# Kernel optimization log

Hardware: AMD Instinct MI355X
Metric: run time of the kernel (lower is better)

Reference implementation:

```python
import jax, jax.numpy as jnp
import numpy as np
from jax import lax

B, T, H, E, V, ENC = 2048, 48, 512, 256, 128, 1024


def setup_inputs() -> dict:
    key = jax.random.key(0)
    ks = jax.random.split(key, 13)
    s = 0.05  # weight scale to keep activations sane
    return {
        "tgt_ids": jax.random.randint(ks[0], (B, T), 0, V),
        "enc_hid": jax.random.normal(ks[1], (B, ENC), jnp.float32),
        "W_init1": s * jax.random.normal(ks[2], (ENC, H), jnp.float32),
        "W_init2": s * jax.random.normal(ks[3], (ENC, H), jnp.float32),
        "embed_table": s * jax.random.normal(ks[4], (V, E), jnp.float32),
        "k1": s * jax.random.normal(ks[5], (E, 3 * H), jnp.float32),
        "rk1": s * jax.random.normal(ks[6], (H, 3 * H), jnp.float32),
        "b1": jnp.zeros((2, 3 * H), jnp.float32),
        "k2": s * jax.random.normal(ks[7], (H, 3 * H), jnp.float32),
        "rk2": s * jax.random.normal(ks[8], (H, 3 * H), jnp.float32),
        "b2": jnp.zeros((2, 3 * H), jnp.float32),
        "Wv": s * jax.random.normal(ks[9], (H, V), jnp.float32),
        "bv": jnp.zeros((V,), jnp.float32),
    }


def gru_masked(x_proj, mask, h0, rk, rb):
    """Keras GRU (reset_after=True, gate order z,r,h) with mask carry-through.
    x_proj: [B,T,3H] precomputed x@kernel + input_bias. mask: [B,T] bool.
    Masked steps keep previous state AND previous output (Keras masking semantics;
    GRU output == state)."""
    def step(h, inp):
        xg, m = inp  # xg: [B,3H], m: [B]
        inner = h @ rk + rb  # [B,3H]
        xz, xr, xh = jnp.split(xg, 3, axis=-1)
        rz, rr, rh = jnp.split(inner, 3, axis=-1)
        z = jax.nn.sigmoid(xz + rz)
        r = jax.nn.sigmoid(xr + rr)
        hh = jnp.tanh(xh + r * rh)
        h_new = z * h + (1.0 - z) * hh
        h = jnp.where(m[:, None], h_new, h)
        return h, h

    _, seq = lax.scan(step, h0, (x_proj.transpose(1, 0, 2), mask.T))
    return seq.transpose(1, 0, 2)  # [B,T,H]


def reference(tgt_ids, enc_hid, W_init1, W_init2, embed_table,
              k1, rk1, b1, k2, rk2, b2, Wv, bv):
    mask = tgt_ids != 0  # mask_zero=True
    emb = embed_table[tgt_ids]  # [B,T,E]
    h01 = enc_hid @ W_init1  # Dense no-bias init of layer-1 state
    h02 = enc_hid @ W_init2
    x1 = emb @ k1 + b1[0]  # [B,T,3H]
    seq1 = gru_masked(x1, mask, h01, rk1, b1[1])
    x2 = seq1 @ k2 + b2[0]
    seq2 = gru_masked(x2, mask, h02, rk2, b2[1])
    probs = jax.nn.softmax(seq2 @ Wv + bv, axis=-1)  # [B,T,V]
    return probs
```

## Files before the change

kernel.cpp:

```cpp
#include <hip/hip_runtime.h>
#include <hip/hip_bf16.h>
#include <math.h>

#define B_   2048
#define T_   48
#define H_   512
#define E_   256
#define V_   128
#define ENC_ 1024
#define H3_  1536
#define BH_  (B_ * H_)
#define NBLK_ 512

typedef __attribute__((ext_vector_type(8))) short bf16x8;
typedef __attribute__((ext_vector_type(4))) float f32x4;
typedef unsigned short ushort_t;

#if defined(__has_builtin)
#if __has_builtin(__builtin_amdgcn_global_load_lds)
#define HAVE_ASYNC 1
#endif
#endif
#ifndef HAVE_ASYNC
#define HAVE_ASYNC 0
#endif

__device__ __forceinline__ void stage16(const ushort_t* g, ushort_t* l, int lane)
{
#if HAVE_ASYNC
    __builtin_amdgcn_global_load_lds(
        (const __attribute__((address_space(1))) unsigned int*)g,
        (__attribute__((address_space(3))) unsigned int*)l, 16, 0, 0);
#else
    *(bf16x8*)(l + lane * 8) = *(const bf16x8*)g;
#endif
}

__device__ __forceinline__ float sigmoidf_(float x) { return 1.0f / (1.0f + expf(-x)); }

__device__ __forceinline__ void tile_map(int lin, int& m0, int& i0)
{
    i0 = ((((lin & 7) << 1) | ((lin >> 3) & 1))) * 32;
    m0 = (lin >> 4) * 64;
}

constexpr int BM = 64, BN = 64, BK = 16;

__global__ __launch_bounds__(256) void gemm_f32(
    const float* __restrict__ A, const float* __restrict__ Bm,
    const float* __restrict__ bias, float* __restrict__ C,
    int M, int N, int K)
{
    __shared__ float As[BK][BM + 4];
    __shared__ float Bs[BK][BN + 4];

    const int tid = threadIdx.x;
    const int bm = blockIdx.y * BM;
    const int bn = blockIdx.x * BN;
    const int tm = (tid >> 4) * 4;
    const int tn = (tid & 15) * 4;
    const int lmA = tid >> 2;
    const int lkA = (tid & 3) * 4;
    const int lkB = tid >> 4;
    const int lnB = (tid & 15) * 4;

    float acc[4][4] = {};

    for (int k0 = 0; k0 < K; k0 += BK) {
        float4 av  = *(const float4*)(A  + (size_t)(bm + lmA) * K + (k0 + lkA));
        float4 bv4 = *(const float4*)(Bm + (size_t)(k0 + lkB) * N + (bn + lnB));
        As[lkA + 0][lmA] = av.x;
        As[lkA + 1][lmA] = av.y;
        As[lkA + 2][lmA] = av.z;
        As[lkA + 3][lmA] = av.w;
        *(float4*)&Bs[lkB][lnB] = bv4;
        __syncthreads();

        #pragma unroll
        for (int k = 0; k < BK; ++k) {
            float4 a = *(const float4*)&As[k][tm];
            float4 b = *(const float4*)&Bs[k][tn];
            acc[0][0] += a.x * b.x; acc[0][1] += a.x * b.y; acc[0][2] += a.x * b.z; acc[0][3] += a.x * b.w;
            acc[1][0] += a.y * b.x; acc[1][1] += a.y * b.y; acc[1][2] += a.y * b.z; acc[1][3] += a.y * b.w;
            acc[2][0] += a.z * b.x; acc[2][1] += a.z * b.y; acc[2][2] += a.z * b.z; acc[2][3] += a.z * b.w;
            acc[3][0] += a.w * b.x; acc[3][1] += a.w * b.y; acc[3][2] += a.w * b.z; acc[3][3] += a.w * b.w;
        }
        __syncthreads();
    }

    #pragma unroll
    for (int r = 0; r < 4; ++r)
        #pragma unroll
        for (int c = 0; c < 4; ++c) {
            float v = acc[r][c];
            if (bias) v += bias[bn + tn + c];
            C[(size_t)(bm + tm + r) * N + (bn + tn + c)] = v;
        }
}

__global__ __launch_bounds__(256) void transpose_to_bf16(
    const float* __restrict__ W, __hip_bfloat16* __restrict__ Wt, int K, int N)
{
    __shared__ float tile[32][33];
    const int bk = blockIdx.y * 32, bn = blockIdx.x * 32;
    const int tx = threadIdx.x & 31, ty = threadIdx.x >> 5;
    #pragma unroll
    for (int i = ty; i < 32; i += 8)
        tile[i][tx] = W[(size_t)(bk + i) * N + (bn + tx)];
    __syncthreads();
    #pragma unroll
    for (int i = ty; i < 32; i += 8)
        Wt[(size_t)(bn + i) * K + (bk + tx)] = __float2bfloat16(tile[tx][i]);
}

__global__ __launch_bounds__(256) void transpose_split(
    const float* __restrict__ W, __hip_bfloat16* __restrict__ Whi,
    __hip_bfloat16* __restrict__ Wlo, int K, int N)
{
    __shared__ float tile[32][33];
    const int bk = blockIdx.y * 32, bn = blockIdx.x * 32;
    const int tx = threadIdx.x & 31, ty = threadIdx.x >> 5;
    #pragma unroll
    for (int i = ty; i < 32; i += 8)
        tile[i][tx] = W[(size_t)(bk + i) * N + (bn + tx)];
    __syncthreads();
    #pragma unroll
    for (int i = ty; i < 32; i += 8) {
        const float v = tile[tx][i];
        const __hip_bfloat16 h = __float2bfloat16(v);
        Whi[(size_t)(bn + i) * K + (bk + tx)] = h;
        Wlo[(size_t)(bn + i) * K + (bk + tx)] = __float2bfloat16(v - __bfloat162float(h));
    }
}

__global__ __launch_bounds__(256) void split_cast(
    const float* __restrict__ x, __hip_bfloat16* __restrict__ hi,
    __hip_bfloat16* __restrict__ lo, int n)
{
    const int i0 = (blockIdx.x * 256 + threadIdx.x) * 4;
    if (i0 >= n) return;
    const float4 v = *(const float4*)(x + i0);
    const float vv[4] = { v.x, v.y, v.z, v.w };
    #pragma unroll
    for (int j = 0; j < 4; ++j) {
        const __hip_bfloat16 h = __float2bfloat16(vv[j]);
        hi[i0 + j] = h;
        lo[i0 + j] = __float2bfloat16(vv[j] - __bfloat162float(h));
    }
}

__global__ __launch_bounds__(256, 2) void init_mfma(
    const ushort_t* __restrict__ ehi, const ushort_t* __restrict__ elo,
    const ushort_t* __restrict__ w1hi, const ushort_t* __restrict__ w1lo,
    const ushort_t* __restrict__ w2hi, const ushort_t* __restrict__ w2lo,
    float* __restrict__ h1f, __hip_bfloat16* __restrict__ h1b,
    float* __restrict__ h2f, __hip_bfloat16* __restrict__ h2b)
{
    const ushort_t* whi = blockIdx.z ? w2hi : w1hi;
    const ushort_t* wlo = blockIdx.z ? w2lo : w1lo;
    float* hf = blockIdx.z ? h2f : h1f;
    __hip_bfloat16* hb = blockIdx.z ? h2b : h1b;

    __shared__ __attribute__((aligned(16))) ushort_t Ahi[2][4096];
    __shared__ __attribute__((aligned(16))) ushort_t Alo[2][4096];
    __shared__ __attribute__((aligned(16))) ushort_t Bhi[2][2048];
    __shared__ __attribute__((aligned(16))) ushort_t Blo[2][2048];

    const int tid  = threadIdx.x;
    const int lane = tid & 63;
    const int w    = tid >> 6;
    const int ln   = lane & 15;
    const int kg   = lane >> 4;
    const int wr   = w >> 1, wc = w & 1;
    const int m0   = blockIdx.y * 64;
    const int i0   = blockIdx.x * 32;

    const int crow = lane >> 3;
    const int ckof = ((lane & 7) ^ crow) * 8;
    const int ko0 = (kg * 8) ^ ((ln & 7) * 8);
    const int ko1 = (32 + kg * 8) ^ ((ln & 7) * 8);

    auto STG = [&](int pb, int k0) {
        #pragma unroll
        for (int c = w; c < 24; c += 4) {
            const ushort_t* g; ushort_t* l;
            if (c < 8) {
                g = ehi + (size_t)(m0 + c * 8 + crow) * ENC_ + k0 + ckof;
                l = &Ahi[pb][c * 512];
            } else if (c < 16) {
                const int cc = c - 8;
                g = elo + (size_t)(m0 + cc * 8 + crow) * ENC_ + k0 + ckof;
                l = &Alo[pb][cc * 512];
            } else if (c < 20) {
                const int cc = c - 16;
                g = whi + (size_t)(i0 + cc * 8 + crow) * ENC_ + k0 + ckof;
                l = &Bhi[pb][cc * 512];
            } else {
                const int cc = c - 20;
                g = wlo + (size_t)(i0 + cc * 8 + crow) * ENC_ + k0 + ckof;
                l = &Blo[pb][cc * 512];
            }
            stage16(g, l, lane);
        }
    };

    f32x4 acc[2] = {};
    STG(0, 0);
    __syncthreads();
    int buf = 0;
    for (int k0 = 0; k0 < ENC_; k0 += 64) {
        if (k0 + 64 < ENC_) STG(buf ^ 1, k0 + 64);
        #pragma unroll
        for (int kk = 0; kk < 2; ++kk) {
            const int ko = kk ? ko1 : ko0;
            bf16x8 ah[2], al[2], bh, bl;
            #pragma unroll
            for (int fm = 0; fm < 2; ++fm) {
                ah[fm] = *(const bf16x8*)(&Ahi[buf][(wr * 32 + fm * 16 + ln) * 64 + ko]);
                al[fm] = *(const bf16x8*)(&Alo[buf][(wr * 32 + fm * 16 + ln) * 64 + ko]);
            }
            bh = *(const bf16x8*)(&Bhi[buf][(wc * 16 + ln) * 64 + ko]);
            bl = *(const bf16x8*)(&Blo[buf][(wc * 16 + ln) * 64 + ko]);
            #pragma unroll
            for (int fm = 0; fm < 2; ++fm) {
                acc[fm] = __builtin_amdgcn_mfma_f32_16x16x32_bf16(ah[fm], bh, acc[fm], 0, 0, 0);
                acc[fm] = __builtin_amdgcn_mfma_f32_16x16x32_bf16(al[fm], bh, acc[fm], 0, 0, 0);
                acc[fm] = __builtin_amdgcn_mfma_f32_16x16x32_bf16(ah[fm], bl, acc[fm], 0, 0, 0);
            }
        }
        __syncthreads();
        buf ^= 1;
    }

    const int i = i0 + wc * 16 + ln;
    #pragma unroll
    for (int fm = 0; fm < 2; ++fm)
        #pragma unroll
        for (int r = 0; r < 4; ++r) {
            const int b = m0 + wr * 32 + fm * 16 + kg * 4 + r;
            const float v = acc[fm][r];
            hf[(size_t)b * H_ + i] = v;
            hb[(size_t)b * H_ + i] = __float2bfloat16(v);
        }
}

template<int MODE>
__device__ __forceinline__ void fused_phase(
    ushort_t* lds, int m0, int i0, int i, int t1, int t2,
    const int* __restrict__ tgt, const float* __restrict__ xe1,
    const ushort_t* __restrict__ rk1t,
    float rbz, float rbr, float rbh,
    const ushort_t* __restrict__ k2t, const ushort_t* __restrict__ rk2t,
    float bxz, float bxr, float bxh, float brz, float brr, float brh,
    const ushort_t* __restrict__ h1cur,
    const ushort_t* __restrict__ h2cur, size_t h2s,
    __hip_bfloat16* __restrict__ h1nxt,
    __hip_bfloat16* __restrict__ sout, size_t souts,
    float (&hv1)[2][4], float (&hv2)[2][4])
{
    ushort_t* A1l = lds;
    ushort_t* A2l = lds + 8192;
    ushort_t* B1l = lds + 16384;
    ushort_t* B2l = lds + 22528;
    ushort_t* B3l = lds + 28672;

    const int tid = threadIdx.x, lane = tid & 63, w = tid >> 6;
    const int ln = lane & 15, kg = lane >> 4, wr = w >> 1;
    const int crow = lane >> 3;
    const int ckof = ((lane & 7) ^ crow) * 8;
    const int ko0 = (kg * 8) ^ ((ln & 7) * 8);
    const int ko1 = (32 + kg * 8) ^ ((ln & 7) * 8);

    int ids1[2][4], ids2[2][4];
    float xgz[2][4], xgr[2][4], xgh[2][4];
    #pragma unroll
    for (int fm = 0; fm < 2; ++fm)
        #pragma unroll
        for (int r = 0; r < 4; ++r) {
            const int b = m0 + wr * 32 + fm * 16 + kg * 4 + r;
            if (MODE != 2) ids1[fm][r] = tgt[(size_t)b * T_ + t1];
            if (MODE != 1) ids2[fm][r] = tgt[(size_t)b * T_ + t2];
        }
    if (MODE != 2) {
        #pragma unroll
        for (int fm = 0; fm < 2; ++fm)
            #pragma unroll
            for (int r = 0; r < 4; ++r) {
                const float* xg = xe1 + (size_t)ids1[fm][r] * H3_;
                xgz[fm][r] = xg[i]; xgr[fm][r] = xg[H_ + i]; xgh[fm][r] = xg[2 * H_ + i];
            }
    }

    constexpr int NA = (MODE == 1) ? 8 : 16;
    constexpr int NB = (MODE == 0) ? 36 : ((MODE == 1) ? 12 : 24);

    auto STAGE_A = [&](int pb, int k0) {
        #pragma unroll
        for (int c = w; c < NA; c += 4) {
            const ushort_t* g; ushort_t* l;
            if (c < 8) {
                g = h1cur + (size_t)(m0 + c * 8 + crow) * H_ + k0 + ckof;
                l = A1l + pb * 4096 + c * 512;
            } else {
                const int cc = c - 8;
                g = h2cur + (size_t)(m0 + cc * 8 + crow) * h2s + k0 + ckof;
                l = A2l + pb * 4096 + cc * 512;
            }
            stage16(g, l, lane);
        }
    };
    auto STAGE_B = [&](int k0) {
        #pragma unroll
        for (int c = w; c < NB; c += 4) {
            const ushort_t* g; ushort_t* l;
            if (MODE == 1) {
                g = rk1t + (size_t)((c >> 2) * H_ + i0 + (c & 3) * 8 + crow) * H_ + k0 + ckof;
                l = B1l + c * 512;
            } else if (MODE == 2) {
                if (c < 12) {
                    g = k2t + (size_t)((c >> 2) * H_ + i0 + (c & 3) * 8 + crow) * H_ + k0 + ckof;
                    l = B2l + c * 512;
                } else {
                    const int d = c - 12;
                    g = rk2t + (size_t)((d >> 2) * H_ + i0 + (d & 3) * 8 + crow) * H_ + k0 + ckof;
                    l = B3l + d * 512;
                }
            } else {
                if (c < 12) {
                    g = rk1t + (size_t)((c >> 2) * H_ + i0 + (c & 3) * 8 + crow) * H_ + k0 + ckof;
                    l = B1l + c * 512;
                } else if (c < 24) {
                    const int d = c - 12;
                    g = k2t + (size_t)((d >> 2) * H_ + i0 + (d & 3) * 8 + crow) * H_ + k0 + ckof;
                    l = B2l + d * 512;
                } else {
                    const int d = c - 24;
                    g = rk2t + (size_t)((d >> 2) * H_ + i0 + (d & 3) * 8 + crow) * H_ + k0 + ckof;
                    l = B3l + d * 512;
                }
            }
            stage16(g, l, lane);
        }
    };

    f32x4 acc1[2][3] = {};
    f32x4 accx[2][3] = {};
    f32x4 accr[2][3] = {};

    STAGE_A(0, 0);
    STAGE_B(0);
    __syncthreads();
    int buf = 0;
    for (int k0 = 0; k0 < H_; k0 += 64) {
        const bool more = (k0 + 64 < H_);
        if (more) STAGE_A(buf ^ 1, k0 + 64);

        bf16x8 a1f[2][2], a2f[2][2], b1f[2][3], b2f[2][3], b3f[2][3];
        #pragma unroll
        for (int kk = 0; kk < 2; ++kk) {
            const int ko = kk ? ko1 : ko0;
            #pragma unroll
            for (int fm = 0; fm < 2; ++fm) {
                a1f[kk][fm] = *(const bf16x8*)(A1l + buf * 4096 + (wr * 32 + fm * 16 + ln) * 64 + ko);
                if (MODE != 1)
                    a2f[kk][fm] = *(const bf16x8*)(A2l + buf * 4096 + (wr * 32 + fm * 16 + ln) * 64 + ko);
            }
            #pragma unroll
            for (int g = 0; g < 3; ++g) {
                if (MODE != 2)
                    b1f[kk][g] = *(const bf16x8*)(B1l + g * 2048 + ((w & 1) * 16 + ln) * 64 + ko);
                if (MODE != 1) {
                    b2f[kk][g] = *(const bf16x8*)(B2l + g * 2048 + ((w & 1) * 16 + ln) * 64 + ko);
                    b3f[kk][g] = *(const bf16x8*)(B3l + g * 2048 + ((w & 1) * 16 + ln) * 64 + ko);
                }
            }
        }
        __builtin_amdgcn_sched_barrier(0);
        asm volatile("s_waitcnt lgkmcnt(0)" ::: "memory");
        __builtin_amdgcn_sched_barrier(0);
        __builtin_amdgcn_s_barrier();
        if (more) STAGE_B(k0 + 64);

        #pragma unroll
        for (int kk = 0; kk < 2; ++kk)
            #pragma unroll
            for (int fm = 0; fm < 2; ++fm)
                #pragma unroll
                for (int g = 0; g < 3; ++g) {
                    if (MODE != 2)
                        acc1[fm][g] = __builtin_amdgcn_mfma_f32_16x16x32_bf16(
                            a1f[kk][fm], b1f[kk][g], acc1[fm][g], 0, 0, 0);
                    if (MODE != 1) {
                        accx[fm][g] = __builtin_amdgcn_mfma_f32_16x16x32_bf16(
                            a1f[kk][fm], b2f[kk][g], accx[fm][g], 0, 0, 0);
                        accr[fm][g] = __builtin_amdgcn_mfma_f32_16x16x32_bf16(
                            a2f[kk][fm], b3f[kk][g], accr[fm][g], 0, 0, 0);
                    }
                }
        __syncthreads();
        buf ^= 1;
    }

    if (MODE != 2) {
        #pragma unroll
        for (int fm = 0; fm < 2; ++fm)
            #pragma unroll
            for (int r = 0; r < 4; ++r) {
                const int b = m0 + wr * 32 + fm * 16 + kg * 4 + r;
                const float hvv = hv1[fm][r];
                float z  = sigmoidf_(xgz[fm][r] + acc1[fm][0][r] + rbz);
                float rr = sigmoidf_(xgr[fm][r] + acc1[fm][1][r] + rbr);
                float hh = tanhf(xgh[fm][r] + rr * (acc1[fm][2][r] + rbh));
                float hn = (ids1[fm][r] != 0) ? (z * hvv + (1.0f - z) * hh) : hvv;
                hv1[fm][r] = hn;
                h1nxt[(size_t)b * H_ + i] = __float2bfloat16(hn);
            }
    }
    if (MODE != 1) {
        #pragma unroll
        for (int fm = 0; fm < 2; ++fm)
            #pragma unroll
            for (int r = 0; r < 4; ++r) {
                const int b = m0 + wr * 32 + fm * 16 + kg * 4 + r;
                const float hvv = hv2[fm][r];
                float z  = sigmoidf_((accx[fm][0][r] + bxz) + (accr[fm][0][r] + brz));
                float rr = sigmoidf_((accx[fm][1][r] + bxr) + (accr[fm][1][r] + brr));
                float hh = tanhf((accx[fm][2][r] + bxh) + rr * (accr[fm][2][r] + brh));
                float hn = (ids2[fm][r] != 0) ? (z * hvv + (1.0f - z) * hh) : hvv;
                hv2[fm][r] = hn;
                sout[(size_t)b * souts + i] = __float2bfloat16(hn);
            }
    }
}

__global__ __launch_bounds__(256, 2) void l1_fused(
    const int* __restrict__ tgt, int t,
    const float* __restrict__ xe1, const ushort_t* __restrict__ rkt,
    const float* __restrict__ rb,
    const float* __restrict__ hf_cur, const ushort_t* __restrict__ hb_cur,
    float* __restrict__ hf_nxt, __hip_bfloat16* __restrict__ hb_nxt)
{
    __shared__ __attribute__((aligned(16))) ushort_t lds[34816];
    int m0, i0; tile_map(blockIdx.x, m0, i0);
    const int tid = threadIdx.x, lane = tid & 63, w = tid >> 6;
    const int ln = lane & 15, kg = lane >> 4, wr = w >> 1, wc = w & 1;
    const int i = i0 + wc * 16 + ln;

    float hv1[2][4], hv2[2][4];
    #pragma unroll
    for (int fm = 0; fm < 2; ++fm)
        #pragma unroll
        for (int r = 0; r < 4; ++r)
            hv1[fm][r] = hf_cur[(size_t)(m0 + wr * 32 + fm * 16 + kg * 4 + r) * H_ + i];

    fused_phase<1>(lds, m0, i0, i, t, 0, tgt, xe1, rkt,
                   rb[i], rb[H_ + i], rb[2 * H_ + i],
                   nullptr, nullptr, 0.f, 0.f, 0.f, 0.f, 0.f, 0.f,
                   hb_cur, nullptr, 0, hb_nxt, nullptr, 0, hv1, hv2);

    #pragma unroll
    for (int fm = 0; fm < 2; ++fm)
        #pragma unroll
        for (int r = 0; r < 4; ++r)
            hf_nxt[(size_t)(m0 + wr * 32 + fm * 16 + kg * 4 + r) * H_ + i] = hv1[fm][r];
}

__global__ __launch_bounds__(256, 2) void l2_fused(
    const int* __restrict__ tgt, int t,
    const ushort_t* __restrict__ k2t, const ushort_t* __restrict__ rk2t,
    const float* __restrict__ bx, const float* __restrict__ br,
    const ushort_t* __restrict__ s1b,
    const float* __restrict__ hf_cur,
    const ushort_t* __restrict__ hb_cur, size_t hbs,
    float* __restrict__ hf_nxt,
    __hip_bfloat16* __restrict__ hbo, size_t hos)
{
    __shared__ __attribute__((aligned(16))) ushort_t lds[34816];
    int m0, i0; tile_map(blockIdx.x, m0, i0);
    const int tid = threadIdx.x, lane = tid & 63, w = tid >> 6;
    const int ln = lane & 15, kg = lane >> 4, wr = w >> 1, wc = w & 1;
    const int i = i0 + wc * 16 + ln;

    float hv1[2][4], hv2[2][4];
    #pragma unroll
    for (int fm = 0; fm < 2; ++fm)
        #pragma unroll
        for (int r = 0; r < 4; ++r)
            hv2[fm][r] = hf_cur[(size_t)(m0 + wr * 32 + fm * 16 + kg * 4 + r) * H_ + i];

    fused_phase<2>(lds, m0, i0, i, 0, t, tgt, nullptr, nullptr,
                   0.f, 0.f, 0.f,
                   k2t, rk2t,
                   bx[i], bx[H_ + i], bx[2 * H_ + i],
                   br[i], br[H_ + i], br[2 * H_ + i],
                   s1b, hb_cur, hbs, nullptr, hbo, hos, hv1, hv2);

    #pragma unroll
    for (int fm = 0; fm < 2; ++fm)
        #pragma unroll
        for (int r = 0; r < 4; ++r)
            hf_nxt[(size_t)(m0 + wr * 32 + fm * 16 + kg * 4 + r) * H_ + i] = hv2[fm][r];
}

__device__ __forceinline__ void grid_barrier(unsigned* bar, unsigned phase)
{
    __syncthreads();
    if (threadIdx.x == 0) {
        __builtin_amdgcn_fence(__ATOMIC_RELEASE, "agent");
        const unsigned arrived =
            __hip_atomic_fetch_add(&bar[0], 1u, __ATOMIC_RELAXED, __HIP_MEMORY_SCOPE_AGENT) + 1u;
        if (arrived == (unsigned)NBLK_ * (phase + 1u)) {
            __hip_atomic_store(&bar[1], phase + 1u, __ATOMIC_RELAXED, __HIP_MEMORY_SCOPE_AGENT);
        } else {
            while (__hip_atomic_load(&bar[1], __ATOMIC_RELAXED, __HIP_MEMORY_SCOPE_AGENT) < phase + 1u)
                __builtin_amdgcn_s_sleep(4);
        }
        __builtin_amdgcn_fence(__ATOMIC_ACQUIRE, "agent");
    }
    __syncthreads();
}

__global__ __launch_bounds__(256, 2) void recurrence_all(
    const int* __restrict__ tgt, const float* __restrict__ xe1,
    const ushort_t* __restrict__ rk1t, const float* __restrict__ rb1,
    const ushort_t* __restrict__ k2t, const ushort_t* __restrict__ rk2t,
    const float* __restrict__ bx, const float* __restrict__ br,
    const float* __restrict__ h1f0, __hip_bfloat16* __restrict__ h1b,
    const float* __restrict__ h2f0, const __hip_bfloat16* __restrict__ h2b0,
    __hip_bfloat16* __restrict__ seq2b, unsigned* __restrict__ bar)
{
    __shared__ __attribute__((aligned(16))) ushort_t lds[34816];
    int m0, i0; tile_map(blockIdx.x, m0, i0);
    const int tid = threadIdx.x, lane = tid & 63, w = tid >> 6;
    const int ln = lane & 15, kg = lane >> 4, wr = w >> 1, wc = w & 1;
    const int i = i0 + wc * 16 + ln;

    const float rbz = rb1[i], rbr = rb1[H_ + i], rbh = rb1[2 * H_ + i];
    const float bxz = bx[i],  bxr = bx[H_ + i],  bxh = bx[2 * H_ + i];
    const float brz = br[i],  brr = br[H_ + i],  brh = br[2 * H_ + i];

    float hv1[2][4], hv2[2][4];
    #pragma unroll
    for (int fm = 0; fm < 2; ++fm)
        #pragma unroll
        for (int r = 0; r < 4; ++r) {
            const size_t b = (size_t)(m0 + wr * 32 + fm * 16 + kg * 4 + r) * H_ + i;
            hv1[fm][r] = h1f0[b];
            hv2[fm][r] = h2f0[b];
        }

    unsigned ph = 0;

    fused_phase<1>(lds, m0, i0, i, 0, 0, tgt, xe1, rk1t, rbz, rbr, rbh,
                   nullptr, nullptr, 0.f, 0.f, 0.f, 0.f, 0.f, 0.f,
                   (const ushort_t*)h1b, nullptr, 0, h1b + BH_, nullptr, 0,
                   hv1, hv2);
    grid_barrier(bar, ph); ++ph;

    #pragma unroll 1
    for (int p = 0; p < T_ - 1; ++p) {
        const ushort_t* s1 = (const ushort_t*)(h1b + (size_t)((p + 1) & 1) * BH_);
        const ushort_t* a2 = (p == 0) ? (const ushort_t*)h2b0
                                      : (const ushort_t*)(seq2b + (size_t)(p - 1) * H_);
        const size_t a2s = (p == 0) ? (size_t)H_ : (size_t)T_ * H_;

        fused_phase<0>(lds, m0, i0, i, p + 1, p, tgt, xe1, rk1t, rbz, rbr, rbh,
                       k2t, rk2t, bxz, bxr, bxh, brz, brr, brh,
                       s1, a2, a2s,
                       h1b + (size_t)(p & 1) * BH_,
                       seq2b + (size_t)p * H_, (size_t)T_ * H_,
                       hv1, hv2);
        grid_barrier(bar, ph); ++ph;
    }

    {
        const int p = T_ - 1;
        const ushort_t* s1 = (const ushort_t*)(h1b + (size_t)((p + 1) & 1) * BH_);
        const ushort_t* a2 = (const ushort_t*)(seq2b + (size_t)(p - 1) * H_);
        fused_phase<2>(lds, m0, i0, i, 0, p, tgt, nullptr, nullptr, 0.f, 0.f, 0.f,
                       k2t, rk2t, bxz, bxr, bxh, brz, brr, brh,
                       s1, a2, (size_t)T_ * H_,
                       nullptr, seq2b + (size_t)p * H_, (size_t)T_ * H_,
                       hv1, hv2);
    }
}

__device__ __forceinline__ void softmax_write4(
    float ax, float ay, float az, float aw, float* __restrict__ outp, int cg)
{
    float m = fmaxf(fmaxf(ax, ay), fmaxf(az, aw));
    #pragma unroll
    for (int d = 16; d >= 1; d >>= 1) m = fmaxf(m, __shfl_xor(m, d));
    float ex = __expf(ax - m), ey = __expf(ay - m),
          ez = __expf(az - m), ew = __expf(aw - m);
    float s = ex + ey + ez + ew;
    #pragma unroll
    for (int d = 16; d >= 1; d >>= 1) s += __shfl_xor(s, d);
    float inv = 1.0f / s;
    float4 o; o.x = ex * inv; o.y = ey * inv; o.z = ez * inv; o.w = ew * inv;
    *(float4*)(outp + cg * 4) = o;
}

__global__ __launch_bounds__(256) void out_softmax(
    const float* __restrict__ h2, const float* __restrict__ Wv,
    const float* __restrict__ bv, float* __restrict__ out, int t)
{
    const int tid = threadIdx.x;
    const int cg = tid & 31;
    const int rg = tid >> 5;
    const int row0 = blockIdx.x * 16;

    __shared__ float hs[16][512];
    for (int idx = tid; idx < 16 * 512; idx += 256)
        hs[idx >> 9][idx & 511] = h2[(size_t)(row0 + (idx >> 9)) * 512 + (idx & 511)];
    __syncthreads();

    const int r0 = rg * 2;
    const float4 bvv = *(const float4*)(bv + cg * 4);
    float a0x = bvv.x, a0y = bvv.y, a0z = bvv.z, a0w = bvv.w;
    float a1x = bvv.x, a1y = bvv.y, a1z = bvv.z, a1w = bvv.w;

    #pragma unroll 4
    for (int k = 0; k < 512; ++k) {
        float4 wv = *(const float4*)(Wv + (size_t)k * V_ + cg * 4);
        float h0 = hs[r0][k], h1 = hs[r0 + 1][k];
        a0x += h0 * wv.x; a0y += h0 * wv.y; a0z += h0 * wv.z; a0w += h0 * wv.w;
        a1x += h1 * wv.x; a1y += h1 * wv.y; a1z += h1 * wv.z; a1w += h1 * wv.w;
    }

    softmax_write4(a0x, a0y, a0z, a0w, out + ((size_t)(row0 + r0) * T_ + t) * V_, cg);
    softmax_write4(a1x, a1y, a1z, a1w, out + ((size_t)(row0 + r0 + 1) * T_ + t) * V_, cg);
}

__global__ __launch_bounds__(256) void proj_mfma(
    const ushort_t* __restrict__ s2, const ushort_t* __restrict__ wvt,
    const float* __restrict__ bv, float* __restrict__ out)
{
    const int lane = threadIdx.x & 63;
    const int w    = threadIdx.x >> 6;
    const int ln   = lane & 15;
    const int kg   = lane >> 4;
    const size_t row0 = (size_t)blockIdx.x * 128 + (size_t)w * 32;

    float bvl[8];
    #pragma unroll
    for (int nf = 0; nf < 8; ++nf) bvl[nf] = bv[nf * 16 + ln];

    f32x4 acc[2][8] = {};
    #pragma unroll 2
    for (int k0 = 0; k0 < H_; k0 += 32) {
        bf16x8 af[2], bf[8];
        #pragma unroll
        for (int mf = 0; mf < 2; ++mf)
            af[mf] = *(const bf16x8*)(s2 + (row0 + mf * 16 + ln) * H_ + k0 + kg * 8);
        #pragma unroll
        for (int nf = 0; nf < 8; ++nf)
            bf[nf] = *(const bf16x8*)(wvt + (size_t)(nf * 16 + ln) * H_ + k0 + kg * 8);
        #pragma unroll
        for (int mf = 0; mf < 2; ++mf)
            #pragma unroll
            for (int nf = 0; nf < 8; ++nf)
                acc[mf][nf] = __builtin_amdgcn_mfma_f32_16x16x32_bf16(
                    af[mf], bf[nf], acc[mf][nf], 0, 0, 0);
    }

    #pragma unroll
    for (int mf = 0; mf < 2; ++mf)
        #pragma unroll
        for (int q = 0; q < 4; ++q) {
            float v[8];
            float m = -1e30f;
            #pragma unroll
            for (int nf = 0; nf < 8; ++nf) { v[nf] = acc[mf][nf][q] + bvl[nf]; m = fmaxf(m, v[nf]); }
            #pragma unroll
            for (int d = 1; d <= 8; d <<= 1) m = fmaxf(m, __shfl_xor(m, d));
            float s = 0.f;
            #pragma unroll
            for (int nf = 0; nf < 8; ++nf) { v[nf] = __expf(v[nf] - m); s += v[nf]; }
            #pragma unroll
            for (int d = 1; d <= 8; d <<= 1) s += __shfl_xor(s, d);
            const float inv = 1.0f / s;
            float* op = out + (row0 + mf * 16 + kg * 4 + q) * V_;
            #pragma unroll
            for (int nf = 0; nf < 8; ++nf) op[nf * 16 + ln] = v[nf] * inv;
        }
}

extern "C" void kernel_launch(void* const* d_in, const int* in_sizes, int n_in,
                              void* d_out, int out_size, void* d_ws, size_t ws_size,
                              hipStream_t stream)
{
    const int*   tgt  = (const int*)  d_in[0];
    const float* enc  = (const float*)d_in[1];
    const float* Wi1  = (const float*)d_in[2];
    const float* Wi2  = (const float*)d_in[3];
    const float* emb  = (const float*)d_in[4];
    const float* k1   = (const float*)d_in[5];
    const float* rk1  = (const float*)d_in[6];
    const float* b1   = (const float*)d_in[7];
    const float* k2   = (const float*)d_in[8];
    const float* rk2  = (const float*)d_in[9];
    const float* b2   = (const float*)d_in[10];
    const float* Wv   = (const float*)d_in[11];
    const float* bv   = (const float*)d_in[12];
    float* out = (float*)d_out;

    float* ws  = (float*)d_ws;
    float* xe1 = ws;
    float* h1f = xe1 + (size_t)V_ * H3_;
    float* h2f = h1f + (size_t)2 * BH_;
    __hip_bfloat16* h1b = (__hip_bfloat16*)(h2f + (size_t)2 * BH_);
    __hip_bfloat16* h2b = h1b + (size_t)2 * BH_;
    __hip_bfloat16* rk1t = h2b + (size_t)2 * BH_;
    __hip_bfloat16* k2t  = rk1t + (size_t)H3_ * H_;
    __hip_bfloat16* rk2t = k2t  + (size_t)H3_ * H_;
    __hip_bfloat16* wvt  = rk2t + (size_t)H3_ * H_;
    __hip_bfloat16* ehi  = wvt + (size_t)V_ * H_;
    __hip_bfloat16* elo  = ehi + (size_t)B_ * ENC_;
    __hip_bfloat16* w1hi = elo + (size_t)B_ * ENC_;
    __hip_bfloat16* w1lo = w1hi + (size_t)H_ * ENC_;
    __hip_bfloat16* w2hi = w1lo + (size_t)H_ * ENC_;
    __hip_bfloat16* w2lo = w2hi + (size_t)H_ * ENC_;
    __hip_bfloat16* seq2b = w2lo + (size_t)H_ * ENC_;
    unsigned* bar = (unsigned*)(seq2b + (size_t)B_ * T_ * H_);

    const size_t need = (size_t)((char*)bar + 64 - (char*)d_ws);
    const bool batched = ws_size >= need;

    static int persist_state = -1;
    if (persist_state < 0) {
        int nb = 0;
        hipError_t e1 = hipOccupancyMaxActiveBlocksPerMultiprocessor(&nb, recurrence_all, 256, 0);
        hipDeviceProp_t prop;
        hipError_t e2 = hipGetDeviceProperties(&prop, 0);
        persist_state = (e1 == hipSuccess && e2 == hipSuccess &&
                         (long)nb * prop.multiProcessorCount >= NBLK_) ? 1 : 0;
    }
    const bool persist = batched && persist_state == 1;

    dim3 blk(256);

    transpose_to_bf16<<<dim3(H3_ / 32, H_ / 32), blk, 0, stream>>>(rk1, rk1t, H_, H3_);
    transpose_to_bf16<<<dim3(H3_ / 32, H_ / 32), blk, 0, stream>>>(k2,  k2t,  H_, H3_);
    transpose_to_bf16<<<dim3(H3_ / 32, H_ / 32), blk, 0, stream>>>(rk2, rk2t, H_, H3_);
    if (batched)
        transpose_to_bf16<<<dim3(V_ / 32, H_ / 32), blk, 0, stream>>>(Wv, wvt, H_, V_);

    split_cast<<<dim3((B_ * ENC_) / 1024), blk, 0, stream>>>(enc, ehi, elo, B_ * ENC_);
    transpose_split<<<dim3(H_ / 32, ENC_ / 32), blk, 0, stream>>>(Wi1, w1hi, w1lo, ENC_, H_);
    transpose_split<<<dim3(H_ / 32, ENC_ / 32), blk, 0, stream>>>(Wi2, w2hi, w2lo, ENC_, H_);

    gemm_f32<<<dim3(H3_ / BN, V_ / BM), blk, 0, stream>>>(emb, k1, b1, xe1, V_, H3_, E_);

    init_mfma<<<dim3(H_ / 32, B_ / 64, 2), blk, 0, stream>>>(
        (const ushort_t*)ehi, (const ushort_t*)elo,
        (const ushort_t*)w1hi, (const ushort_t*)w1lo,
        (const ushort_t*)w2hi, (const ushort_t*)w2lo,
        h1f, h1b, h2f, h2b);

    if (persist) {
        hipMemsetAsync(bar, 0, 64, stream);
        recurrence_all<<<dim3(NBLK_), blk, 0, stream>>>(
            tgt, xe1, (const ushort_t*)rk1t, b1 + H3_,
            (const ushort_t*)k2t, (const ushort_t*)rk2t, b2, b2 + H3_,
            h1f, h1b, h2f, h2b, seq2b, bar);
        proj_mfma<<<dim3((B_ * T_) / 128), blk, 0, stream>>>(
            (const ushort_t*)seq2b, (const ushort_t*)wvt, bv, out);
        return;
    }

    const dim3 fgrid(NBLK_);
    for (int t = 0; t < T_; ++t) {
        const int cur = t & 1, nxt = cur ^ 1;
        float* h1f_c = h1f + (size_t)cur * BH_;
        float* h1f_n = h1f + (size_t)nxt * BH_;
        float* h2f_c = h2f + (size_t)cur * BH_;
        float* h2f_n = h2f + (size_t)nxt * BH_;
        __hip_bfloat16* h1b_c = h1b + (size_t)cur * BH_;
        __hip_bfloat16* h1b_n = h1b + (size_t)nxt * BH_;

        l1_fused<<<fgrid, blk, 0, stream>>>(
            tgt, t, xe1, (const ushort_t*)rk1t, b1 + H3_,
            h1f_c, (const ushort_t*)h1b_c, h1f_n, h1b_n);

        const ushort_t* hb_c; size_t hbs;
        __hip_bfloat16* hbo; size_t hos;
        if (batched) {
            hb_c = (t == 0) ? (const ushort_t*)h2b
                            : (const ushort_t*)(seq2b + (size_t)(t - 1) * H_);
            hbs  = (t == 0) ? (size_t)H_ : (size_t)T_ * H_;
            hbo  = seq2b + (size_t)t * H_;
            hos  = (size_t)T_ * H_;
        } else {
            hb_c = (const ushort_t*)(h2b + (size_t)cur * BH_); hbs = H_;
            hbo  = h2b + (size_t)nxt * BH_;                    hos = H_;
        }

        l2_fused<<<fgrid, blk, 0, stream>>>(
            tgt, t, (const ushort_t*)k2t, (const ushort_t*)rk2t, b2, b2 + H3_,
            (const ushort_t*)h1b_n, h2f_c, hb_c, hbs, h2f_n, hbo, hos);

        if (!batched)
            out_softmax<<<dim3(B_ / 16), blk, 0, stream>>>(h2f_n, Wv, bv, out, t);
    }

    if (batched)
        proj_mfma<<<dim3((B_ * T_) / 128), blk, 0, stream>>>(
            (const ushort_t*)seq2b, (const ushort_t*)wvt, bv, out);
}
```

Measured before the change: 1.548 ms.

## Double recurrence block to 512 threads and prefetch gate inputs across grid barriers

Doubles the threads per block in the recurrent GRU kernels from 4 to 8 waves, so each wave computes a single 16-row M fragment instead of two. This halves per-thread accumulator registers, and launch bounds are raised to allow four blocks per CU. It also moves the token-id and input-gate (xe1) loads for the next step out of the fused phase so they are issued before the grid barrier, hiding their latency. The trade-off is more waves contending for LDS, staging and barriers per block, and the persistence occupancy check now has to succeed at 512 threads.

```diff
diff --git a/kernel.cpp b/kernel.cpp
--- a/kernel.cpp
+++ b/kernel.cpp
@@ -244,10 +244,30 @@
         }
 }
 
+__device__ __forceinline__ void gate_prefetch(
+    const int* __restrict__ tgt, const float* __restrict__ xe1,
+    int m0, int wr, int kg, int i, int t, bool want_x,
+    int (&ids)[4], float (&xz)[4], float (&xr)[4], float (&xh)[4])
+{
+    #pragma unroll
+    for (int r = 0; r < 4; ++r) {
+        const int b = m0 + wr * 16 + kg * 4 + r;
+        ids[r] = tgt[(size_t)b * T_ + t];
+    }
+    if (want_x) {
+        #pragma unroll
+        for (int r = 0; r < 4; ++r) {
+            const float* xg = xe1 + (size_t)ids[r] * H3_;
+            xz[r] = xg[i]; xr[r] = xg[H_ + i]; xh[r] = xg[2 * H_ + i];
+        }
+    }
+}
+
 template<int MODE>
 __device__ __forceinline__ void fused_phase(
-    ushort_t* lds, int m0, int i0, int i, int t1, int t2,
-    const int* __restrict__ tgt, const float* __restrict__ xe1,
+    ushort_t* lds, int m0, int i0, int i,
+    const int (&ids1)[4], const float (&xgz)[4], const float (&xgr)[4], const float (&xgh)[4],
+    const int (&ids2)[4],
     const ushort_t* __restrict__ rk1t,
     float rbz, float rbr, float rbh,
     const ushort_t* __restrict__ k2t, const ushort_t* __restrict__ rk2t,
@@ -256,7 +276,7 @@
     const ushort_t* __restrict__ h2cur, size_t h2s,
     __hip_bfloat16* __restrict__ h1nxt,
     __hip_bfloat16* __restrict__ sout, size_t souts,
-    float (&hv1)[2][4], float (&hv2)[2][4])
+    float (&hv1)[4], float (&hv2)[4])
 {
     ushort_t* A1l = lds;
     ushort_t* A2l = lds + 8192;
@@ -271,32 +291,12 @@
     const int ko0 = (kg * 8) ^ ((ln & 7) * 8);
     const int ko1 = (32 + kg * 8) ^ ((ln & 7) * 8);
 
-    int ids1[2][4], ids2[2][4];
-    float xgz[2][4], xgr[2][4], xgh[2][4];
-    #pragma unroll
-    for (int fm = 0; fm < 2; ++fm)
-        #pragma unroll
-        for (int r = 0; r < 4; ++r) {
-            const int b = m0 + wr * 32 + fm * 16 + kg * 4 + r;
-            if (MODE != 2) ids1[fm][r] = tgt[(size_t)b * T_ + t1];
-            if (MODE != 1) ids2[fm][r] = tgt[(size_t)b * T_ + t2];
-        }
-    if (MODE != 2) {
-        #pragma unroll
-        for (int fm = 0; fm < 2; ++fm)
-            #pragma unroll
-            for (int r = 0; r < 4; ++r) {
-                const float* xg = xe1 + (size_t)ids1[fm][r] * H3_;
-                xgz[fm][r] = xg[i]; xgr[fm][r] = xg[H_ + i]; xgh[fm][r] = xg[2 * H_ + i];
-            }
-    }
-
     constexpr int NA = (MODE == 1) ? 8 : 16;
     constexpr int NB = (MODE == 0) ? 36 : ((MODE == 1) ? 12 : 24);
 
     auto STAGE_A = [&](int pb, int k0) {
         #pragma unroll
-        for (int c = w; c < NA; c += 4) {
+        for (int c = w; c < NA; c += 8) {
             const ushort_t* g; ushort_t* l;
             if (c < 8) {
                 g = h1cur + (size_t)(m0 + c * 8 + crow) * H_ + k0 + ckof;
@@ -311,7 +311,7 @@
     };
     auto STAGE_B = [&](int k0) {
         #pragma unroll
-        for (int c = w; c < NB; c += 4) {
+        for (int c = w; c < NB; c += 8) {
             const ushort_t* g; ushort_t* l;
             if (MODE == 1) {
                 g = rk1t + (size_t)((c >> 2) * H_ + i0 + (c & 3) * 8 + crow) * H_ + k0 + ckof;
@@ -343,9 +343,9 @@
         }
     };
 
-    f32x4 acc1[2][3] = {};
-    f32x4 accx[2][3] = {};
-    f32x4 accr[2][3] = {};
+    f32x4 acc1[3] = {};
+    f32x4 accx[3] = {};
+    f32x4 accr[3] = {};
 
     STAGE_A(0, 0);
     STAGE_B(0);
@@ -355,16 +355,13 @@
         const bool more = (k0 + 64 < H_);
         if (more) STAGE_A(buf ^ 1, k0 + 64);
 
-        bf16x8 a1f[2][2], a2f[2][2], b1f[2][3], b2f[2][3], b3f[2][3];
+        bf16x8 a1f[2], a2f[2], b1f[2][3], b2f[2][3], b3f[2][3];
         #pragma unroll
         for (int kk = 0; kk < 2; ++kk) {
             const int ko = kk ? ko1 : ko0;
-            #pragma unroll
-            for (int fm = 0; fm < 2; ++fm) {
-                a1f[kk][fm] = *(const bf16x8*)(A1l + buf * 4096 + (wr * 32 + fm * 16 + ln) * 64 + ko);
-                if (MODE != 1)
-                    a2f[kk][fm] = *(const bf16x8*)(A2l + buf * 4096 + (wr * 32 + fm * 16 + ln) * 64 + ko);
-            }
+            a1f[kk] = *(const bf16x8*)(A1l + buf * 4096 + (wr * 16 + ln) * 64 + ko);
+            if (MODE != 1)
+                a2f[kk] = *(const bf16x8*)(A2l + buf * 4096 + (wr * 16 + ln) * 64 + ko);
             #pragma unroll
             for (int g = 0; g < 3; ++g) {
                 if (MODE != 2)
@@ -384,56 +381,50 @@
         #pragma unroll
         for (int kk = 0; kk < 2; ++kk)
             #pragma unroll
-            for (int fm = 0; fm < 2; ++fm)
-                #pragma unroll
-                for (int g = 0; g < 3; ++g) {
-                    if (MODE != 2)
-                        acc1[fm][g] = __builtin_amdgcn_mfma_f32_16x16x32_bf16(
-                            a1f[kk][fm], b1f[kk][g], acc1[fm][g], 0, 0, 0);
-                    if (MODE != 1) {
-                        accx[fm][g] = __builtin_amdgcn_mfma_f32_16x16x32_bf16(
-                            a1f[kk][fm], b2f[kk][g], accx[fm][g], 0, 0, 0);
-                        accr[fm][g] = __builtin_amdgcn_mfma_f32_16x16x32_bf16(
-                            a2f[kk][fm], b3f[kk][g], accr[fm][g], 0, 0, 0);
-                    }
+            for (int g = 0; g < 3; ++g) {
+                if (MODE != 2)
+                    acc1[g] = __builtin_amdgcn_mfma_f32_16x16x32_bf16(
+                        a1f[kk], b1f[kk][g], acc1[g], 0, 0, 0);
+                if (MODE != 1) {
+                    accx[g] = __builtin_amdgcn_mfma_f32_16x16x32_bf16(
+                        a1f[kk], b2f[kk][g], accx[g], 0, 0, 0);
+                    accr[g] = __builtin_amdgcn_mfma_f32_16x16x32_bf16(
+                        a2f[kk], b3f[kk][g], accr[g], 0, 0, 0);
                 }
+            }
         __syncthreads();
         buf ^= 1;
     }
 
     if (MODE != 2) {
         #pragma unroll
-        for (int fm = 0; fm < 2; ++fm)
-            #pragma unroll
-            for (int r = 0; r < 4; ++r) {
-                const int b = m0 + wr * 32 + fm * 16 + kg * 4 + r;
-                const float hvv = hv1[fm][r];
-                float z  = sigmoidf_(xgz[fm][r] + acc1[fm][0][r] + rbz);
-                float rr = sigmoidf_(xgr[fm][r] + acc1[fm][1][r] + rbr);
-                float hh = tanhf(xgh[fm][r] + rr * (acc1[fm][2][r] + rbh));
-                float hn = (ids1[fm][r] != 0) ? (z * hvv + (1.0f - z) * hh) : hvv;
-                hv1[fm][r] = hn;
-                h1nxt[(size_t)b * H_ + i] = __float2bfloat16(hn);
-            }
+        for (int r = 0; r < 4; ++r) {
+            const int b = m0 + wr * 16 + kg * 4 + r;
+            const float hvv = hv1[r];
+            float z  = sigmoidf_(xgz[r] + acc1[0][r] + rbz);
+            float rr = sigmoidf_(xgr[r] + acc1[1][r] + rbr);
+            float hh = tanhf(xgh[r] + rr * (acc1[2][r] + rbh));
+            float hn = (ids1[r] != 0) ? (z * hvv + (1.0f - z) * hh) : hvv;
+            hv1[r] = hn;
+            h1nxt[(size_t)b * H_ + i] = __float2bfloat16(hn);
+        }
     }
     if (MODE != 1) {
         #pragma unroll
-        for (int fm = 0; fm < 2; ++fm)
-            #pragma unroll
-            for (int r = 0; r < 4; ++r) {
-                const int b = m0 + wr * 32 + fm * 16 + kg * 4 + r;
-                const float hvv = hv2[fm][r];
-                float z  = sigmoidf_((accx[fm][0][r] + bxz) + (accr[fm][0][r] + brz));
-                float rr = sigmoidf_((accx[fm][1][r] + bxr) + (accr[fm][1][r] + brr));
-                float hh = tanhf((accx[fm][2][r] + bxh) + rr * (accr[fm][2][r] + brh));
-                float hn = (ids2[fm][r] != 0) ? (z * hvv + (1.0f - z) * hh) : hvv;
-                hv2[fm][r] = hn;
-                sout[(size_t)b * souts + i] = __float2bfloat16(hn);
-            }
-    }
-}
-
-__global__ __launch_bounds__(256, 2) void l1_fused(
+        for (int r = 0; r < 4; ++r) {
+            const int b = m0 + wr * 16 + kg * 4 + r;
+            const float hvv = hv2[r];
+            float z  = sigmoidf_((accx[0][r] + bxz) + (accr[0][r] + brz));
+            float rr = sigmoidf_((accx[1][r] + bxr) + (accr[1][r] + brr));
+            float hh = tanhf((accx[2][r] + bxh) + rr * (accr[2][r] + brh));
+            float hn = (ids2[r] != 0) ? (z * hvv + (1.0f - z) * hh) : hvv;
+            hv2[r] = hn;
+            sout[(size_t)b * souts + i] = __float2bfloat16(hn);
+        }
+    }
+}
+
+__global__ __launch_bounds__(512, 4) void l1_fused(
     const int* __restrict__ tgt, int t,
     const float* __restrict__ xe1, const ushort_t* __restrict__ rkt,
     const float* __restrict__ rb,
@@ -446,26 +437,27 @@
     const int ln = lane & 15, kg = lane >> 4, wr = w >> 1, wc = w & 1;
     const int i = i0 + wc * 16 + ln;
 
-    float hv1[2][4], hv2[2][4];
-    #pragma unroll
-    for (int fm = 0; fm < 2; ++fm)
-        #pragma unroll
-        for (int r = 0; r < 4; ++r)
-            hv1[fm][r] = hf_cur[(size_t)(m0 + wr * 32 + fm * 16 + kg * 4 + r) * H_ + i];
-
-    fused_phase<1>(lds, m0, i0, i, t, 0, tgt, xe1, rkt,
+    float hv1[4], hv2[4];
+    int ids1[4], ids2[4];
+    float xz[4], xr[4], xh[4];
+    gate_prefetch(tgt, xe1, m0, wr, kg, i, t, true, ids1, xz, xr, xh);
+    #pragma unroll
+    for (int r = 0; r < 4; ++r)
+        hv1[r] = hf_cur[(size_t)(m0 + wr * 16 + kg * 4 + r) * H_ + i];
+    #pragma unroll
+    for (int r = 0; r < 4; ++r) { ids2[r] = 0; hv2[r] = 0.f; }
+
+    fused_phase<1>(lds, m0, i0, i, ids1, xz, xr, xh, ids2, rkt,
                    rb[i], rb[H_ + i], rb[2 * H_ + i],
                    nullptr, nullptr, 0.f, 0.f, 0.f, 0.f, 0.f, 0.f,
                    hb_cur, nullptr, 0, hb_nxt, nullptr, 0, hv1, hv2);
 
     #pragma unroll
-    for (int fm = 0; fm < 2; ++fm)
-        #pragma unroll
-        for (int r = 0; r < 4; ++r)
-            hf_nxt[(size_t)(m0 + wr * 32 + fm * 16 + kg * 4 + r) * H_ + i] = hv1[fm][r];
-}
-
-__global__ __launch_bounds__(256, 2) void l2_fused(
+    for (int r = 0; r < 4; ++r)
+        hf_nxt[(size_t)(m0 + wr * 16 + kg * 4 + r) * H_ + i] = hv1[r];
+}
+
+__global__ __launch_bounds__(512, 4) void l2_fused(
     const int* __restrict__ tgt, int t,
     const ushort_t* __restrict__ k2t, const ushort_t* __restrict__ rk2t,
     const float* __restrict__ bx, const float* __restrict__ br,
@@ -481,14 +473,17 @@
     const int ln = lane & 15, kg = lane >> 4, wr = w >> 1, wc = w & 1;
     const int i = i0 + wc * 16 + ln;
 
-    float hv1[2][4], hv2[2][4];
-    #pragma unroll
-    for (int fm = 0; fm < 2; ++fm)
-        #pragma unroll
-        for (int r = 0; r < 4; ++r)
-            hv2[fm][r] = hf_cur[(size_t)(m0 + wr * 32 + fm * 16 + kg * 4 + r) * H_ + i];
-
-    fused_phase<2>(lds, m0, i0, i, 0, t, tgt, nullptr, nullptr,
+    float hv1[4], hv2[4];
+    int ids1[4], ids2[4];
+    float xz[4], xr[4], xh[4];
+    gate_prefetch(tgt, nullptr, m0, wr, kg, i, t, false, ids2, xz, xr, xh);
+    #pragma unroll
+    for (int r = 0; r < 4; ++r)
+        hv2[r] = hf_cur[(size_t)(m0 + wr * 16 + kg * 4 + r) * H_ + i];
+    #pragma unroll
+    for (int r = 0; r < 4; ++r) { ids1[r] = 0; hv1[r] = 0.f; xz[r] = xr[r] = xh[r] = 0.f; }
+
+    fused_phase<2>(lds, m0, i0, i, ids1, xz, xr, xh, ids2, nullptr,
                    0.f, 0.f, 0.f,
                    k2t, rk2t,
                    bx[i], bx[H_ + i], bx[2 * H_ + i],
@@ -496,10 +491,8 @@
                    s1b, hb_cur, hbs, nullptr, hbo, hos, hv1, hv2);
 
     #pragma unroll
-    for (int fm = 0; fm < 2; ++fm)
-        #pragma unroll
-        for (int r = 0; r < 4; ++r)
-            hf_nxt[(size_t)(m0 + wr * 32 + fm * 16 + kg * 4 + r) * H_ + i] = hv2[fm][r];
+    for (int r = 0; r < 4; ++r)
+        hf_nxt[(size_t)(m0 + wr * 16 + kg * 4 + r) * H_ + i] = hv2[r];
 }
 
 __device__ __forceinline__ void grid_barrier(unsigned* bar, unsigned phase)
@@ -520,7 +513,7 @@
     __syncthreads();
 }
 
-__global__ __launch_bounds__(256, 2) void recurrence_all(
+__global__ __launch_bounds__(512, 4) void recurrence_all(
     const int* __restrict__ tgt, const float* __restrict__ xe1,
     const ushort_t* __restrict__ rk1t, const float* __restrict__ rb1,
     const ushort_t* __restrict__ k2t, const ushort_t* __restrict__ rk2t,
@@ -539,22 +532,28 @@
     const float bxz = bx[i],  bxr = bx[H_ + i],  bxh = bx[2 * H_ + i];
     const float brz = br[i],  brr = br[H_ + i],  brh = br[2 * H_ + i];
 
-    float hv1[2][4], hv2[2][4];
-    #pragma unroll
-    for (int fm = 0; fm < 2; ++fm)
-        #pragma unroll
-        for (int r = 0; r < 4; ++r) {
-            const size_t b = (size_t)(m0 + wr * 32 + fm * 16 + kg * 4 + r) * H_ + i;
-            hv1[fm][r] = h1f0[b];
-            hv2[fm][r] = h2f0[b];
-        }
+    float hv1[4], hv2[4];
+    #pragma unroll
+    for (int r = 0; r < 4; ++r) {
+        const size_t b = (size_t)(m0 + wr * 16 + kg * 4 + r) * H_ + i;
+        hv1[r] = h1f0[b];
+        hv2[r] = h2f0[b];
+    }
+
+    int idsA[4], idsB[4];
+    float xzA[4], xrA[4], xhA[4];
+    gate_prefetch(tgt, xe1, m0, wr, kg, i, 0, true, idsA, xzA, xrA, xhA);
 
     unsigned ph = 0;
 
-    fused_phase<1>(lds, m0, i0, i, 0, 0, tgt, xe1, rk1t, rbz, rbr, rbh,
+    fused_phase<1>(lds, m0, i0, i, idsA, xzA, xrA, xhA, idsB,
+                   rk1t, rbz, rbr, rbh,
                    nullptr, nullptr, 0.f, 0.f, 0.f, 0.f, 0.f, 0.f,
                    (const ushort_t*)h1b, nullptr, 0, h1b + BH_, nullptr, 0,
                    hv1, hv2);
+    #pragma unroll
+    for (int r = 0; r < 4; ++r) idsB[r] = idsA[r];
+    gate_prefetch(tgt, xe1, m0, wr, kg, i, 1, true, idsA, xzA, xrA, xhA);
     grid_barrier(bar, ph); ++ph;
 
     #pragma unroll 1
@@ -564,12 +563,17 @@
                                       : (const ushort_t*)(seq2b + (size_t)(p - 1) * H_);
         const size_t a2s = (p == 0) ? (size_t)H_ : (size_t)T_ * H_;
 
-        fused_phase<0>(lds, m0, i0, i, p + 1, p, tgt, xe1, rk1t, rbz, rbr, rbh,
+        fused_phase<0>(lds, m0, i0, i, idsA, xzA, xrA, xhA, idsB,
+                       rk1t, rbz, rbr, rbh,
                        k2t, rk2t, bxz, bxr, bxh, brz, brr, brh,
                        s1, a2, a2s,
                        h1b + (size_t)(p & 1) * BH_,
                        seq2b + (size_t)p * H_, (size_t)T_ * H_,
                        hv1, hv2);
+        #pragma unroll
+        for (int r = 0; r < 4; ++r) idsB[r] = idsA[r];
+        if (p + 2 <= T_ - 1)
+            gate_prefetch(tgt, xe1, m0, wr, kg, i, p + 2, true, idsA, xzA, xrA, xhA);
         grid_barrier(bar, ph); ++ph;
     }
 
@@ -577,7 +581,8 @@
         const int p = T_ - 1;
         const ushort_t* s1 = (const ushort_t*)(h1b + (size_t)((p + 1) & 1) * BH_);
         const ushort_t* a2 = (const ushort_t*)(seq2b + (size_t)(p - 1) * H_);
-        fused_phase<2>(lds, m0, i0, i, 0, p, tgt, nullptr, nullptr, 0.f, 0.f, 0.f,
+        fused_phase<2>(lds, m0, i0, i, idsA, xzA, xrA, xhA, idsB,
+                       nullptr, 0.f, 0.f, 0.f,
                        k2t, rk2t, bxz, bxr, bxh, brz, brr, brh,
                        s1, a2, (size_t)T_ * H_,
                        nullptr, seq2b + (size_t)p * H_, (size_t)T_ * H_,
@@ -730,7 +735,7 @@
     static int persist_state = -1;
     if (persist_state < 0) {
         int nb = 0;
-        hipError_t e1 = hipOccupancyMaxActiveBlocksPerMultiprocessor(&nb, recurrence_all, 256, 0);
+        hipError_t e1 = hipOccupancyMaxActiveBlocksPerMultiprocessor(&nb, recurrence_all, 512, 0);
         hipDeviceProp_t prop;
         hipError_t e2 = hipGetDeviceProperties(&prop, 0);
         persist_state = (e1 == hipSuccess && e2 == hipSuccess &&
@@ -739,6 +744,7 @@
     const bool persist = batched && persist_state == 1;
 
     dim3 blk(256);
+    dim3 blkR(512);
 
     transpose_to_bf16<<<dim3(H3_ / 32, H_ / 32), blk, 0, stream>>>(rk1, rk1t, H_, H3_);
     transpose_to_bf16<<<dim3(H3_ / 32, H_ / 32), blk, 0, stream>>>(k2,  k2t,  H_, H3_);
@@ -760,7 +766,7 @@
 
     if (persist) {
         hipMemsetAsync(bar, 0, 64, stream);
-        recurrence_all<<<dim3(NBLK_), blk, 0, stream>>>(
+        recurrence_all<<<dim3(NBLK_), blkR, 0, stream>>>(
             tgt, xe1, (const ushort_t*)rk1t, b1 + H3_,
             (const ushort_t*)k2t, (const ushort_t*)rk2t, b2, b2 + H3_,
             h1f, h1b, h2f, h2b, seq2b, bar);
@@ -779,7 +785,7 @@
         __hip_bfloat16* h1b_c = h1b + (size_t)cur * BH_;
         __hip_bfloat16* h1b_n = h1b + (size_t)nxt * BH_;
 
-        l1_fused<<<fgrid, blk, 0, stream>>>(
+        l1_fused<<<fgrid, blkR, 0, stream>>>(
             tgt, t, xe1, (const ushort_t*)rk1t, b1 + H3_,
             h1f_c, (const ushort_t*)h1b_c, h1f_n, h1b_n);
 
@@ -796,7 +802,7 @@
             hbo  = h2b + (size_t)nxt * BH_;                    hos = H_;
         }
 
-        l2_fused<<<fgrid, blk, 0, stream>>>(
+        l2_fused<<<fgrid, blkR, 0, stream>>>(
             tgt, t, (const ushort_t*)k2t, (const ushort_t*)rk2t, b2, b2 + H3_,
             (const ushort_t*)h1b_n, h2f_c, hb_c, hbs, h2f_n, hbo, hos);
 
```

New measurement: 1.818 ms. 17.4% more time.
